# Performance work log

Measured on AMD Instinct MI355X. Metric: run time of the kernel, lower is better.

The kernel has to match this reference:

```python
import jax, jax.numpy as jnp
import numpy as np

DIM = 1024
NUM_HEADS = 8
HEAD_DIM = 128
MAX_SEQ_LEN = 2048
ATTN_SCALE = 0.12
RMS_EPS = 1.1920929e-07  # torch float32 eps (F.rms_norm default)


def rms_norm(x):
    return x * jax.lax.rsqrt(jnp.mean(jnp.square(x), axis=-1, keepdims=True) + RMS_EPS)


def rope_tables(T):
    # angular_freq: (1/1024)**linspace(0,1,head_dim//4), padded with head_dim//4 zeros -> length head_dim//2
    af = (1.0 / 1024.0) ** np.linspace(0.0, 1.0, HEAD_DIM // 4, dtype=np.float32)
    af = np.concatenate([af, np.zeros(HEAD_DIM // 4, dtype=np.float32)])
    t = np.arange(T, dtype=np.float32)
    theta = np.einsum('i,j->ij', t, af)  # [T, head_dim//2]
    return jnp.asarray(np.cos(theta)), jnp.asarray(np.sin(theta))


def apply_rope(x_BTHD, cos, sin):
    # cos/sin: [T, head_dim//2] -> broadcast [1,T,1,hd//2]
    c = cos[None, :, None, :]
    s = sin[None, :, None, :]
    x1, x2 = jnp.split(x_BTHD, 2, axis=-1)
    y1 = x1 * c + x2 * s
    y2 = -x1 * s + x2 * c
    return jnp.concatenate([y1, y2], axis=-1)


def setup_inputs() -> dict:
    key = jax.random.key(0)
    k1, k2, k3, k4, k5 = jax.random.split(key, 5)
    B, T = 4, 2048
    hdim = NUM_HEADS * HEAD_DIM
    std = 0.5 * DIM ** (-0.5)
    bound = (3.0 ** 0.5) * std
    x = jax.random.normal(k1, (B, T, DIM), dtype=jnp.float32)
    ve = jax.random.normal(k2, (B, T, DIM), dtype=jnp.float32)
    sa_lambdas = jax.random.uniform(k3, (2,), dtype=jnp.float32)
    qkv_w = jax.random.uniform(k4, (3, hdim, DIM), dtype=jnp.float32, minval=-bound, maxval=bound)
    # original inits c_proj to zeros; use small random so the output is non-trivial
    c_proj_weight = jax.random.normal(k5, (DIM, hdim), dtype=jnp.float32) * 0.02
    return {"x": x, "ve": ve, "sa_lambdas": sa_lambdas, "qkv_w": qkv_w,
            "c_proj_weight": c_proj_weight}


def reference(x, ve, sa_lambdas, qkv_w, c_proj_weight):
    B, T, D = x.shape
    H, hd = NUM_HEADS, HEAD_DIM
    Wqkv = qkv_w.reshape(3 * H * hd, D)
    qkv = jnp.einsum('btd,ed->bte', x, Wqkv).reshape(B, T, 3 * H, hd)
    q, k, v = jnp.split(qkv, 3, axis=-2)  # each [B,T,H,hd]
    q, k = rms_norm(q), rms_norm(k)
    cos, sin = rope_tables(T)
    q, k = apply_rope(q, cos, sin), apply_rope(k, cos, sin)
    v = sa_lambdas[0] * v + sa_lambdas[1] * ve.reshape(B, T, H, hd)
    # [B,H,T,T] scores
    attn = jnp.einsum('bqhd,bkhd->bhqk', q, k) * ATTN_SCALE
    causal = jnp.triu(jnp.ones((T, T), dtype=bool), k=1)
    attn = jnp.where(causal[None, None], -jnp.inf, attn)
    attn = jax.nn.softmax(attn, axis=-1)
    y = jnp.einsum('bhqk,bkhd->bqhd', attn, v).reshape(B, T, H * hd)
    return jnp.einsum('bte,de->btd', y, c_proj_weight)
```

## Files before the change

kernel.cpp:

```cpp
#include <hip/hip_runtime.h>

#define DIM 1024
#define NH 8
#define HD 128
#define T_SEQ 2048
#define NTOK 8192
#define QKV_N 3072
#define ATTN_SCALE 0.12f
#define RMS_EPS 1.1920929e-07f

using f32x4  = __attribute__((ext_vector_type(4))) float;
using bf16x8 = __attribute__((ext_vector_type(8))) __bf16;

__device__ __forceinline__ unsigned short f2bf(float f) {
    unsigned int u = __builtin_bit_cast(unsigned int, f);
    u += 0x7fffu + ((u >> 16) & 1u);
    return (unsigned short)(u >> 16);
}
__device__ __forceinline__ float bf2f(unsigned short s) {
    unsigned int u = ((unsigned int)s) << 16;
    return __builtin_bit_cast(float, u);
}

__device__ __forceinline__ void gll16(const void* g, void* l) {
    __builtin_amdgcn_global_load_lds(
        (const __attribute__((address_space(1))) unsigned int*)g,
        (__attribute__((address_space(3))) unsigned int*)l, 16, 0, 0);
}

#define VMCNT(n) asm volatile("s_waitcnt vmcnt(" #n ")" ::: "memory")
#define LGKM0 do { asm volatile("s_waitcnt lgkmcnt(0)" ::: "memory"); \
                   __builtin_amdgcn_sched_barrier(0); } while(0)
#define PH_BAR __builtin_amdgcn_s_barrier()

__global__ __launch_bounds__(256) void cvt_f32_bf16(const float* __restrict__ in,
                                                    unsigned short* __restrict__ out,
                                                    int n4) {
    int i = blockIdx.x * 256 + threadIdx.x;
    if (i < n4) {
        float4 f = ((const float4*)in)[i];
        ushort4 o;
        o.x = f2bf(f.x); o.y = f2bf(f.y); o.z = f2bf(f.z); o.w = f2bf(f.w);
        ((ushort4*)out)[i] = o;
    }
}

__global__ __launch_bounds__(256) void rope_tab(float2* __restrict__ tab) {
    int idx = blockIdx.x * 256 + threadIdx.x;
    int t = idx >> 5, i = idx & 31;
    float th = (float)t * exp2f((float)i * (-10.0f/31.0f));
    float sn, cs;
    sincosf(th, &sn, &cs);
    tab[idx] = make_float2(cs, sn);
}

template<int OUTF32>
__global__ __launch_bounds__(512, 1) void gemm8p(const unsigned short* __restrict__ A,
                                                 const unsigned short* __restrict__ B,
                                                 void* __restrict__ Cout,
                                                 int M, int N, int K, int nbn) {
    __shared__ __align__(16) char smem[139264];
    const int tid  = threadIdx.x;
    const int lane = tid & 63;
    const int w    = tid >> 6;
    const int wm   = w >> 2, wn = w & 3;
    const int lr   = lane & 15, lg = lane >> 4;

    const int chunk = gridDim.x >> 3;
    const int bid2  = (blockIdx.x & 7) * chunk + (blockIdx.x >> 3);
    const int bm = (bid2 / nbn) * 256;
    const int bn = (bid2 % nbn) * 256;

    const int srow = lane >> 3;
    const int scol = ((lane & 7) ^ srow) << 3;
    const int KT = K / 64;

    auto ldsA = [&](int p, int h) -> unsigned short* {
        return (unsigned short*)(smem + p*65536 + h*16384);
    };
    auto ldsB = [&](int p, int h) -> unsigned short* {
        return (unsigned short*)(smem + p*65536 + 32768 + h*16384);
    };
    auto stA = [&](int t, int p, int h) {
        if (t >= KT) return;
        char* dst = (char*)ldsA(p, h);
        #pragma unroll
        for (int i = 0; i < 2; ++i) {
            int c = w*2 + i;
            gll16(&A[(size_t)(bm + h*128 + c*8 + srow)*K + t*64 + scol], dst + c*1024);
        }
    };
    auto stB = [&](int t, int p, int h) {
        if (t >= KT) return;
        char* dst = (char*)ldsB(p, h);
        #pragma unroll
        for (int i = 0; i < 2; ++i) {
            int c = w*2 + i;
            gll16(&B[(size_t)(bn + h*128 + c*8 + srow)*K + t*64 + scol], dst + c*1024);
        }
    };

    f32x4 acc[8][4] = {};
    bf16x8 a[4][2], b0[2][2], b1[2][2];

    auto rdA4 = [&](int p, int qm) {
        const unsigned short* base = ldsA(p, wm);
        #pragma unroll
        for (int m = 0; m < 4; ++m) {
            int row = qm*64 + m*16 + lr;
            int sw = (row & 7) << 3;
            #pragma unroll
            for (int kk = 0; kk < 2; ++kk)
                a[m][kk] = *(const bf16x8*)&base[row*64 + ((kk*32 + lg*8) ^ sw)];
        }
    };
    auto rdB2 = [&](int p, int qn, bf16x8 (*bq)[2]) {
        const unsigned short* base = ldsB(p, wn >> 1);
        #pragma unroll
        for (int n = 0; n < 2; ++n) {
            int row = (wn & 1)*64 + qn*32 + n*16 + lr;
            int sw = (row & 7) << 3;
            #pragma unroll
            for (int kk = 0; kk < 2; ++kk)
                bq[n][kk] = *(const bf16x8*)&base[row*64 + ((kk*32 + lg*8) ^ sw)];
        }
    };
    auto mm = [&](int qm, int qn, bf16x8 (*bq)[2]) {
        __builtin_amdgcn_s_setprio(1);
        #pragma unroll
        for (int m = 0; m < 4; ++m)
            #pragma unroll
            for (int n = 0; n < 2; ++n)
                #pragma unroll
                for (int kk = 0; kk < 2; ++kk)
                    acc[qm*4+m][qn*2+n] =
                        __builtin_amdgcn_mfma_f32_16x16x32_bf16(a[m][kk], bq[n][kk],
                                                                acc[qm*4+m][qn*2+n], 0, 0, 0);
        __builtin_amdgcn_s_setprio(0);
    };

    stB(0, 0, 0); stB(0, 0, 1); stA(0, 0, 0); stA(0, 0, 1);
    stB(1, 1, 0); stB(1, 1, 1);
    VMCNT(4);
    PH_BAR;

    for (int i = 0; i < KT/2; ++i) {
        const int t0 = 2*i;
        const bool steady = (i + 1 < KT/2);
        rdA4(0, 0); rdB2(0, 0, b0);
        stA(t0+1, 1, 0);
        PH_BAR; LGKM0;
        mm(0, 0, b0);
        PH_BAR;
        rdB2(0, 1, b1);
        stA(t0+1, 1, 1);
        PH_BAR; LGKM0;
        mm(0, 1, b1);
        PH_BAR;
        rdA4(0, 1);
        stB(t0+2, 0, 0);
        PH_BAR; LGKM0;
        mm(1, 0, b0);
        PH_BAR;
        stB(t0+2, 0, 1);
        if (steady) { VMCNT(4); } else { VMCNT(0); }
        PH_BAR;
        mm(1, 1, b1);
        PH_BAR;
        rdA4(1, 0); rdB2(1, 0, b0);
        stA(t0+2, 0, 0);
        PH_BAR; LGKM0;
        mm(0, 0, b0);
        PH_BAR;
        rdB2(1, 1, b1);
        stA(t0+2, 0, 1);
        PH_BAR; LGKM0;
        mm(0, 1, b1);
        PH_BAR;
        rdA4(1, 1);
        stB(t0+3, 1, 0);
        PH_BAR; LGKM0;
        mm(1, 0, b0);
        PH_BAR;
        stB(t0+3, 1, 1);
        if (steady) { VMCNT(4); } else { VMCNT(0); }
        PH_BAR;
        mm(1, 1, b1);
        PH_BAR;
    }

    __syncthreads();
    float* sc = (float*)(smem + (size_t)w * 17408);
    #pragma unroll
    for (int f = 0; f < 2; ++f) {
        #pragma unroll
        for (int m = 0; m < 4; ++m)
            #pragma unroll
            for (int n = 0; n < 4; ++n)
                #pragma unroll
                for (int r = 0; r < 4; ++r)
                    sc[(m*16 + lg*4 + r)*68 + n*16 + lr] = acc[f*4+m][n][r];
        if (OUTF32) {
            float* C = (float*)Cout;
            #pragma unroll
            for (int rnd = 0; rnd < 16; ++rnd) {
                int g = rnd*64 + lane;
                int row = g >> 4, c4 = (g & 15) * 4;
                float4 v = *(float4*)&sc[row*68 + c4];
                *(float4*)&C[(size_t)(bm + wm*128 + f*64 + row)*N + bn + wn*64 + c4] = v;
            }
        } else {
            unsigned short* C = (unsigned short*)Cout;
            #pragma unroll
            for (int rnd = 0; rnd < 8; ++rnd) {
                int g = rnd*64 + lane;
                int row = g >> 3, c8 = (g & 7) * 8;
                float4 v0 = *(float4*)&sc[row*68 + c8];
                float4 v1 = *(float4*)&sc[row*68 + c8 + 4];
                uint4 o;
                o.x = f2bf(v0.x) | ((unsigned)f2bf(v0.y) << 16);
                o.y = f2bf(v0.z) | ((unsigned)f2bf(v0.w) << 16);
                o.z = f2bf(v1.x) | ((unsigned)f2bf(v1.y) << 16);
                o.w = f2bf(v1.z) | ((unsigned)f2bf(v1.w) << 16);
                *(uint4*)&C[(size_t)(bm + wm*128 + f*64 + row)*N + bn + wn*64 + c8] = o;
            }
        }
    }
}

#define SLOT_A 32768
#define SLOT_SZ 49152

template<int OUTF32>
__global__ __launch_bounds__(512, 1) void gemm256(const unsigned short* __restrict__ A,
                                                  const unsigned short* __restrict__ B,
                                                  void* __restrict__ Cout,
                                                  int M, int N, int K, int nbn) {
    __shared__ __align__(16) char smem[147456];
    const int tid  = threadIdx.x;
    const int lane = tid & 63;
    const int w    = tid >> 6;
    const int wm   = w >> 1, wn = w & 1;
    const int lr   = lane & 15, lg = lane >> 4;
    const int xsw  = (lr & 7) << 3;

    const int chunk = gridDim.x >> 3;
    const int bid2  = (blockIdx.x & 7) * chunk + (blockIdx.x >> 3);
    const int m0 = (bid2 / nbn) * 256;
    const int n0 = (bid2 % nbn) * 128;

    const int rsub = lane >> 3;
    const int csw  = ((lane & 7) ^ rsub) << 3;

    char* s0 = smem;
    char* s1 = smem + SLOT_SZ;
    char* s2 = smem + 2*SLOT_SZ;

    auto stage = [&](int kt, char* slot) {
        const int kb = kt * 64;
        #pragma unroll
        for (int i = 0; i < 4; ++i) {
            int c = w*4 + i;
            gll16(&A[(size_t)(m0 + c*8 + rsub)*K + kb + csw], slot + c*1024);
        }
        #pragma unroll
        for (int i = 0; i < 2; ++i) {
            int c = w*2 + i;
            gll16(&B[(size_t)(n0 + c*8 + rsub)*K + kb + csw], slot + SLOT_A + c*1024);
        }
    };

    f32x4 acc[4][4] = {};
    const int KT = K / 64;

    stage(0, s0);
    stage(1, s1);
    VMCNT(6);
    __builtin_amdgcn_s_barrier();
    __builtin_amdgcn_sched_barrier(0);

    for (int t = 0; t < KT; ++t) {
        if (t + 2 < KT) stage(t + 2, s2);
        const unsigned short* sA = (const unsigned short*)s0;
        const unsigned short* sB = (const unsigned short*)(s0 + SLOT_A);
        bf16x8 bfr[4][2];
        #pragma unroll
        for (int n = 0; n < 4; ++n)
            #pragma unroll
            for (int kk = 0; kk < 2; ++kk)
                bfr[n][kk] = *(const bf16x8*)&sB[(wn*64 + n*16 + lr)*64 + ((kk*32 + lg*8) ^ xsw)];
        #pragma unroll
        for (int m = 0; m < 4; ++m) {
            bf16x8 af[2];
            #pragma unroll
            for (int kk = 0; kk < 2; ++kk)
                af[kk] = *(const bf16x8*)&sA[(wm*64 + m*16 + lr)*64 + ((kk*32 + lg*8) ^ xsw)];
            __builtin_amdgcn_s_setprio(1);
            #pragma unroll
            for (int n = 0; n < 4; ++n)
                #pragma unroll
                for (int kk = 0; kk < 2; ++kk)
                    acc[m][n] = __builtin_amdgcn_mfma_f32_16x16x32_bf16(af[kk], bfr[n][kk], acc[m][n], 0, 0, 0);
            __builtin_amdgcn_s_setprio(0);
        }
        if (t + 2 < KT) { VMCNT(6); }
        else            { VMCNT(0); }
        __builtin_amdgcn_s_barrier();
        __builtin_amdgcn_sched_barrier(0);
        char* tmp = s0; s0 = s1; s1 = s2; s2 = tmp;
    }

    __syncthreads();
    float* sc = (float*)(smem + (size_t)w * 17408);
    #pragma unroll
    for (int m = 0; m < 4; ++m)
        #pragma unroll
        for (int n = 0; n < 4; ++n)
            #pragma unroll
            for (int r = 0; r < 4; ++r)
                sc[(m*16 + lg*4 + r)*68 + n*16 + lr] = acc[m][n][r];

    if (OUTF32) {
        float* C = (float*)Cout;
        #pragma unroll
        for (int rnd = 0; rnd < 16; ++rnd) {
            int g = rnd*64 + lane;
            int row = g >> 4, c4 = (g & 15) * 4;
            float4 v = *(float4*)&sc[row*68 + c4];
            *(float4*)&C[(size_t)(m0 + wm*64 + row)*N + n0 + wn*64 + c4] = v;
        }
    } else {
        unsigned short* C = (unsigned short*)Cout;
        #pragma unroll
        for (int rnd = 0; rnd < 8; ++rnd) {
            int g = rnd*64 + lane;
            int row = g >> 3, c8 = (g & 7) * 8;
            float4 v0 = *(float4*)&sc[row*68 + c8];
            float4 v1 = *(float4*)&sc[row*68 + c8 + 4];
            uint4 o;
            o.x = f2bf(v0.x) | ((unsigned)f2bf(v0.y) << 16);
            o.y = f2bf(v0.z) | ((unsigned)f2bf(v0.w) << 16);
            o.z = f2bf(v1.x) | ((unsigned)f2bf(v1.y) << 16);
            o.w = f2bf(v1.z) | ((unsigned)f2bf(v1.w) << 16);
            *(uint4*)&C[(size_t)(m0 + wm*64 + row)*N + n0 + wn*64 + c8] = o;
        }
    }
}

__global__ __launch_bounds__(256) void qkv_post(const unsigned short* __restrict__ qkv,
                                                const float2* __restrict__ tab,
                                                unsigned short* __restrict__ qO,
                                                unsigned short* __restrict__ kO) {
    int gw   = (blockIdx.x * 256 + threadIdx.x) >> 6;
    int lane = threadIdx.x & 63;
    int h     = gw & 7;
    int token = gw >> 3;
    int t     = token & (T_SEQ-1);
    int b     = token >> 11;

    const unsigned short* base = qkv + (size_t)token * QKV_N + h*HD;
    float q1 = bf2f(base[lane]),        q2 = bf2f(base[lane+64]);
    float k1 = bf2f(base[1024+lane]),   k2 = bf2f(base[1024+lane+64]);

    float sq = q1*q1 + q2*q2;
    float sk = k1*k1 + k2*k2;
    #pragma unroll
    for (int m = 1; m < 64; m <<= 1) {
        sq += __shfl_xor(sq, m);
        sk += __shfl_xor(sk, m);
    }
    float qs = rsqrtf(sq * (1.0f/128.0f) + RMS_EPS) * (ATTN_SCALE * 1.44269504088896f);
    float ks = rsqrtf(sk * (1.0f/128.0f) + RMS_EPS);
    q1 *= qs; q2 *= qs; k1 *= ks; k2 *= ks;

    float cs = 1.0f, sn = 0.0f;
    if (lane < 32) { float2 cc = tab[t*32 + lane]; cs = cc.x; sn = cc.y; }
    float qy1 =  q1*cs + q2*sn, qy2 = -q1*sn + q2*cs;
    float ky1 =  k1*cs + k2*sn, ky2 = -k1*sn + k2*cs;

    size_t obase = ((size_t)(b*NH + h) * T_SEQ + t) * HD;
    qO[obase + lane]      = f2bf(qy1);
    qO[obase + lane + 64] = f2bf(qy2);
    kO[obase + lane]      = f2bf(ky1);
    kO[obase + lane + 64] = f2bf(ky2);
}

__global__ __launch_bounds__(256) void vmix_t(const unsigned short* __restrict__ qkv,
                                              const float* __restrict__ ve,
                                              const float* __restrict__ lam,
                                              unsigned short* __restrict__ vt) {
    __shared__ unsigned short lT[128*72];
    const int tid = threadIdx.x;
    const int t0  = blockIdx.x * 64;
    const int bh  = blockIdx.y;
    const int b = bh >> 3, h = bh & 7;
    const float l0 = lam[0], l1 = lam[1];

    #pragma unroll
    for (int it = 0; it < 4; ++it) {
        int g  = it*256 + tid;
        int t  = g >> 4;
        int d8 = (g & 15) << 3;
        size_t token = (size_t)b*T_SEQ + t0 + t;
        ushort4 v0 = *(const ushort4*)&qkv[token*QKV_N + 2048 + h*HD + d8];
        ushort4 v1 = *(const ushort4*)&qkv[token*QKV_N + 2048 + h*HD + d8 + 4];
        float4 e0 = *(const float4*)&ve[token*DIM + h*HD + d8];
        float4 e1 = *(const float4*)&ve[token*DIM + h*HD + d8 + 4];
        lT[(d8+0)*72 + t] = f2bf(l0*bf2f(v0.x) + l1*e0.x);
        lT[(d8+1)*72 + t] = f2bf(l0*bf2f(v0.y) + l1*e0.y);
        lT[(d8+2)*72 + t] = f2bf(l0*bf2f(v0.z) + l1*e0.z);
        lT[(d8+3)*72 + t] = f2bf(l0*bf2f(v0.w) + l1*e0.w);
        lT[(d8+4)*72 + t] = f2bf(l0*bf2f(v1.x) + l1*e1.x);
        lT[(d8+5)*72 + t] = f2bf(l0*bf2f(v1.y) + l1*e1.y);
        lT[(d8+6)*72 + t] = f2bf(l0*bf2f(v1.z) + l1*e1.z);
        lT[(d8+7)*72 + t] = f2bf(l0*bf2f(v1.w) + l1*e1.w);
    }
    __syncthreads();
    #pragma unroll
    for (int it = 0; it < 4; ++it) {
        int g  = it*256 + tid;
        int d  = g >> 3;
        int t8 = (g & 7) << 3;
        uint4 pk = *(const uint4*)&lT[d*72 + t8];
        *(uint4*)&vt[((size_t)bh*HD + d)*T_SEQ + t0 + t8] = pk;
    }
}

__global__ __launch_bounds__(256, 2) void attn_fwd(const unsigned short* __restrict__ Q,
                                                   const unsigned short* __restrict__ K,
                                                   const unsigned short* __restrict__ Vt,
                                                   unsigned short* __restrict__ Y) {
    __shared__ unsigned short lK[2][64*128];
    __shared__ unsigned short lV[2][128*64];
    __shared__ unsigned short lP[4][16*64];

    const int tid  = threadIdx.x;
    const int lane = tid & 63;
    const int w    = tid >> 6;
    const int lr   = lane & 15, lg = lane >> 4;

    const int lin = blockIdx.y * 16 + blockIdx.x;
    const int bh  = (lin & 7)*4 + ((lin >> 3) & 3);
    const int p   = lin >> 5;
    const int qtA = p, qtB = 31 - p;

    const unsigned short* Qg = Q  + (size_t)bh * T_SEQ * HD;
    const unsigned short* Kg = K  + (size_t)bh * T_SEQ * HD;
    const unsigned short* Vg = Vt + (size_t)bh * HD * T_SEQ;
    const int q0A = qtA*64 + w*16;
    const int q0B = qtB*64 + w*16;

    auto stage = [&](int kt, int s) {
        const int kbase = kt * 64;
        #pragma unroll
        for (int i = 0; i < 4; ++i) {
            int c = w*4 + i;
            int row = c*4 + (lane >> 4);
            int col = ((lane & 15) << 3) ^ ((row & 7) << 3);
            gll16(&Kg[(size_t)(kbase + row)*HD + col], &lK[s][c*512]);
        }
        #pragma unroll
        for (int i = 0; i < 4; ++i) {
            int c = w*4 + i;
            int row = c*8 + (lane >> 3);
            int col = ((lane & 7) << 3) ^ ((row & 7) << 3);
            gll16(&Vg[(size_t)row*T_SEQ + kbase + col], &lV[s][c*512]);
        }
    };

    bf16x8 qfA[4], qfB[4];
    #pragma unroll
    for (int kk = 0; kk < 4; ++kk) {
        qfA[kk] = *(const bf16x8*)&Qg[(size_t)(q0A + lr)*HD + kk*32 + lg*8];
        qfB[kk] = *(const bf16x8*)&Qg[(size_t)(q0B + lr)*HD + kk*32 + lg*8];
    }
    VMCNT(0);
    #pragma unroll
    for (int kk = 0; kk < 4; ++kk)
        asm volatile("" :: "v"(qfA[kk]), "v"(qfB[kk]));

    f32x4 oA[8] = {}, oB[8] = {};
    float psA[4] = {0.f,0.f,0.f,0.f}, psB[4] = {0.f,0.f,0.f,0.f};

    auto passAB = [&](bool diagA, int kbase,
                      const unsigned short* lKc, const unsigned short* lVc) {
        f32x4 sfA[4], sfB[4];
        __builtin_amdgcn_s_setprio(1);
        #pragma unroll
        for (int j = 0; j < 4; ++j) {
            f32x4 sA = {0.f,0.f,0.f,0.f}, sB = {0.f,0.f,0.f,0.f};
            #pragma unroll
            for (int kk = 0; kk < 4; ++kk) {
                bf16x8 kf = *(const bf16x8*)&lKc[(j*16+lr)*128 + ((kk*32 + lg*8) ^ ((lr&7)<<3))];
                sA = __builtin_amdgcn_mfma_f32_16x16x32_bf16(qfA[kk], kf, sA, 0, 0, 0);
                sB = __builtin_amdgcn_mfma_f32_16x16x32_bf16(qfB[kk], kf, sB, 0, 0, 0);
            }
            sfA[j] = sA; sfB[j] = sB;
        }
        __builtin_amdgcn_s_setprio(0);
        if (diagA) {
            #pragma unroll
            for (int j = 0; j < 4; ++j)
                #pragma unroll
                for (int r = 0; r < 4; ++r) {
                    int kcol = kbase + j*16 + lr;
                    int qrow = q0A + lg*4 + r;
                    if (kcol > qrow) sfA[j][r] = -INFINITY;
                }
        }
        #pragma unroll
        for (int j = 0; j < 4; ++j)
            #pragma unroll
            for (int r = 0; r < 4; ++r) {
                float pp = exp2f(sfA[j][r]);
                sfA[j][r] = pp;
                psA[r] += pp;
            }
        asm volatile("" ::: "memory");
        #pragma unroll
        for (int j = 0; j < 4; ++j)
            #pragma unroll
            for (int r = 0; r < 4; ++r) {
                int prow = lg*4 + r;
                lP[w][prow*64 + ((j*16 + lr) ^ ((prow&7)<<3))] = f2bf(sfA[j][r]);
            }
        asm volatile("" ::: "memory");
        bf16x8 pfA[2];
        #pragma unroll
        for (int kk = 0; kk < 2; ++kk)
            pfA[kk] = *(const bf16x8*)&lP[w][lr*64 + ((kk*32 + lg*8) ^ ((lr&7)<<3))];
        #pragma unroll
        for (int j = 0; j < 4; ++j)
            #pragma unroll
            for (int r = 0; r < 4; ++r) {
                float pp = exp2f(sfB[j][r]);
                sfB[j][r] = pp;
                psB[r] += pp;
            }
        asm volatile("" ::: "memory");
        #pragma unroll
        for (int j = 0; j < 4; ++j)
            #pragma unroll
            for (int r = 0; r < 4; ++r) {
                int prow = lg*4 + r;
                lP[w][prow*64 + ((j*16 + lr) ^ ((prow&7)<<3))] = f2bf(sfB[j][r]);
            }
        asm volatile("" ::: "memory");
        bf16x8 pfB[2];
        #pragma unroll
        for (int kk = 0; kk < 2; ++kk)
            pfB[kk] = *(const bf16x8*)&lP[w][lr*64 + ((kk*32 + lg*8) ^ ((lr&7)<<3))];
        #pragma unroll
        for (int n = 0; n < 8; ++n) {
            bf16x8 vf0 = *(const bf16x8*)&lVc[(n*16+lr)*64 + (( 0 + lg*8) ^ ((lr&7)<<3))];
            bf16x8 vf1 = *(const bf16x8*)&lVc[(n*16+lr)*64 + ((32 + lg*8) ^ ((lr&7)<<3))];
            __builtin_amdgcn_s_setprio(1);
            oA[n] = __builtin_amdgcn_mfma_f32_16x16x32_bf16(pfA[0], vf0, oA[n], 0, 0, 0);
            oA[n] = __builtin_amdgcn_mfma_f32_16x16x32_bf16(pfA[1], vf1, oA[n], 0, 0, 0);
            oB[n] = __builtin_amdgcn_mfma_f32_16x16x32_bf16(pfB[0], vf0, oB[n], 0, 0, 0);
            oB[n] = __builtin_amdgcn_mfma_f32_16x16x32_bf16(pfB[1], vf1, oB[n], 0, 0, 0);
            __builtin_amdgcn_s_setprio(0);
        }
    };

    auto pass = [&](bool diag, int kbase,
                    const unsigned short* lKc, const unsigned short* lVc) {
        f32x4 sf[4];
        __builtin_amdgcn_s_setprio(1);
        #pragma unroll
        for (int j = 0; j < 4; ++j) {
            f32x4 s = {0.f,0.f,0.f,0.f};
            #pragma unroll
            for (int kk = 0; kk < 4; ++kk) {
                bf16x8 kf = *(const bf16x8*)&lKc[(j*16+lr)*128 + ((kk*32 + lg*8) ^ ((lr&7)<<3))];
                s = __builtin_amdgcn_mfma_f32_16x16x32_bf16(qfB[kk], kf, s, 0, 0, 0);
            }
            sf[j] = s;
        }
        __builtin_amdgcn_s_setprio(0);
        if (diag) {
            #pragma unroll
            for (int j = 0; j < 4; ++j)
                #pragma unroll
                for (int r = 0; r < 4; ++r) {
                    int kcol = kbase + j*16 + lr;
                    int qrow = q0B + lg*4 + r;
                    if (kcol > qrow) sf[j][r] = -INFINITY;
                }
        }
        #pragma unroll
        for (int j = 0; j < 4; ++j)
            #pragma unroll
            for (int r = 0; r < 4; ++r) {
                float pp = exp2f(sf[j][r]);
                sf[j][r] = pp;
                psB[r] += pp;
            }
        asm volatile("" ::: "memory");
        #pragma unroll
        for (int j = 0; j < 4; ++j)
            #pragma unroll
            for (int r = 0; r < 4; ++r) {
                int prow = lg*4 + r;
                lP[w][prow*64 + ((j*16 + lr) ^ ((prow&7)<<3))] = f2bf(sf[j][r]);
            }
        asm volatile("" ::: "memory");
        bf16x8 pf[2];
        #pragma unroll
        for (int kk = 0; kk < 2; ++kk)
            pf[kk] = *(const bf16x8*)&lP[w][lr*64 + ((kk*32 + lg*8) ^ ((lr&7)<<3))];
        #pragma unroll
        for (int n = 0; n < 8; ++n) {
            bf16x8 vf0 = *(const bf16x8*)&lVc[(n*16+lr)*64 + (( 0 + lg*8) ^ ((lr&7)<<3))];
            bf16x8 vf1 = *(const bf16x8*)&lVc[(n*16+lr)*64 + ((32 + lg*8) ^ ((lr&7)<<3))];
            __builtin_amdgcn_s_setprio(1);
            oB[n] = __builtin_amdgcn_mfma_f32_16x16x32_bf16(pf[0], vf0, oB[n], 0, 0, 0);
            oB[n] = __builtin_amdgcn_mfma_f32_16x16x32_bf16(pf[1], vf1, oB[n], 0, 0, 0);
            __builtin_amdgcn_s_setprio(0);
        }
    };

    stage(0, 0);
    for (int kt = 0; kt <= qtB; ++kt) {
        __builtin_amdgcn_s_barrier();
        const bool pre = (kt + 1 <= qtB);
        if (pre) stage(kt + 1, (kt + 1) & 1);
        if (pre) { VMCNT(8); } else { VMCNT(0); }
        __builtin_amdgcn_sched_barrier(0);
        const int kbase = kt * 64;
        const unsigned short* lKc = lK[kt & 1];
        const unsigned short* lVc = lV[kt & 1];
        if (kt <= qtA) passAB(kt == qtA, kbase, lKc, lVc);
        else           pass(kt == qtB, kbase, lKc, lVc);
    }

    #pragma unroll
    for (int m = 1; m < 16; m <<= 1)
        #pragma unroll
        for (int r = 0; r < 4; ++r) {
            psA[r] += __shfl_xor(psA[r], m);
            psB[r] += __shfl_xor(psB[r], m);
        }
    float riA[4], riB[4];
    #pragma unroll
    for (int r = 0; r < 4; ++r) { riA[r] = 1.0f / psA[r]; riB[r] = 1.0f / psB[r]; }

    const int b = bh >> 3, h = bh & 7;
    #pragma unroll
    for (int n = 0; n < 8; ++n)
        #pragma unroll
        for (int r = 0; r < 4; ++r) {
            int d = n*16 + lr;
            int qrowA = q0A + lg*4 + r;
            int qrowB = q0B + lg*4 + r;
            Y[((size_t)(b*T_SEQ + qrowA))*DIM + h*HD + d] = f2bf(oA[n][r] * riA[r]);
            Y[((size_t)(b*T_SEQ + qrowB))*DIM + h*HD + d] = f2bf(oB[n][r] * riB[r]);
        }
}

extern "C" void kernel_launch(void* const* d_in, const int* in_sizes, int n_in,
                              void* d_out, int out_size, void* d_ws, size_t ws_size,
                              hipStream_t stream) {
    const float* x      = (const float*)d_in[0];
    const float* ve     = (const float*)d_in[1];
    const float* lam    = (const float*)d_in[2];
    const float* qkvw   = (const float*)d_in[3];
    const float* cprojw = (const float*)d_in[4];

    char* ws = (char*)d_ws;
    unsigned short* xb  = (unsigned short*)(ws);
    unsigned short* wqb = (unsigned short*)(ws + 16777216);
    unsigned short* cpb = (unsigned short*)(ws + 23068672);
    unsigned short* qkv = (unsigned short*)(ws + 25165824);
    unsigned short* qa  = (unsigned short*)(ws + 75497472);
    unsigned short* ka  = (unsigned short*)(ws + 92274688);
    unsigned short* vt  = (unsigned short*)(ws + 109051904);
    unsigned short* ya  = (unsigned short*)(ws + 125829120);
    float2* tab = (float2*)(ws);

    cvt_f32_bf16<<<8192, 256, 0, stream>>>(x, xb, 2097152);
    cvt_f32_bf16<<<3072, 256, 0, stream>>>(qkvw, wqb, 786432);
    cvt_f32_bf16<<<1024, 256, 0, stream>>>(cprojw, cpb, 262144);

    gemm8p<0><<<384, 512, 0, stream>>>(xb, wqb, qkv, NTOK, QKV_N, DIM, 12);
    rope_tab<<<256, 256, 0, stream>>>(tab);
    qkv_post<<<16384, 256, 0, stream>>>(qkv, tab, qa, ka);
    vmix_t<<<dim3(32, 32), 256, 0, stream>>>(qkv, ve, lam, vt);
    attn_fwd<<<dim3(16, 32), 256, 0, stream>>>(qa, ka, vt, ya);
    gemm256<1><<<256, 512, 0, stream>>>(ya, cpb, (float*)d_out, NTOK, DIM, DIM, 8);
}
```

Measured before the change: 203.9 us.

## Restructure GEMM pipeline to single-tile stages and transpose attention score layout

The GEMM main loop is reorganised from a two-tile unrolled phase schedule into one K-tile per iteration with double-buffered A fragments. It also allows two blocks per CU via launch bounds and adds a barrier between epilogue halves. The attention kernel computes scores as K·Q^T so each lane holds one query row, which lets P be packed with v_cvt_pk_bf16_f32 into a padded, unswizzled LDS tile. Row sums become a single per-lane accumulator reduced with two shuffles and shared through LDS. The intent is to cut conversion, shuffle and LDS-swizzle overhead, at the risk of more bank conflicts from the padding and register pressure under the new launch bound.

```diff
diff --git a/kernel.cpp b/kernel.cpp
--- a/kernel.cpp
+++ b/kernel.cpp
@@ -21,6 +21,11 @@
     unsigned int u = ((unsigned int)s) << 16;
     return __builtin_bit_cast(float, u);
 }
+__device__ __forceinline__ unsigned int cvtpk(float lo, float hi) {
+    unsigned int r;
+    asm("v_cvt_pk_bf16_f32 %0, %1, %2" : "=v"(r) : "v"(lo), "v"(hi));
+    return r;
+}
 
 __device__ __forceinline__ void gll16(const void* g, void* l) {
     __builtin_amdgcn_global_load_lds(
@@ -29,6 +34,7 @@
 }
 
 #define VMCNT(n) asm volatile("s_waitcnt vmcnt(" #n ")" ::: "memory")
+#define LGKM(n)  asm volatile("s_waitcnt lgkmcnt(" #n ")" ::: "memory")
 #define LGKM0 do { asm volatile("s_waitcnt lgkmcnt(0)" ::: "memory"); \
                    __builtin_amdgcn_sched_barrier(0); } while(0)
 #define PH_BAR __builtin_amdgcn_s_barrier()
@@ -55,7 +61,7 @@
 }
 
 template<int OUTF32>
-__global__ __launch_bounds__(512, 1) void gemm8p(const unsigned short* __restrict__ A,
+__global__ __launch_bounds__(512, 2) void gemm8p(const unsigned short* __restrict__ A,
                                                  const unsigned short* __restrict__ B,
                                                  void* __restrict__ Cout,
                                                  int M, int N, int K, int nbn) {
@@ -71,40 +77,34 @@
     const int bm = (bid2 / nbn) * 256;
     const int bn = (bid2 % nbn) * 256;
 
-    const int srow = lane >> 3;
-    const int scol = ((lane & 7) ^ srow) << 3;
+    const int rsub = lane >> 3;
+    const int csw  = ((lane & 7) ^ rsub) << 3;
     const int KT = K / 64;
 
-    auto ldsA = [&](int p, int h) -> unsigned short* {
-        return (unsigned short*)(smem + p*65536 + h*16384);
-    };
-    auto ldsB = [&](int p, int h) -> unsigned short* {
-        return (unsigned short*)(smem + p*65536 + 32768 + h*16384);
-    };
-    auto stA = [&](int t, int p, int h) {
+    auto stA = [&](int t, int h) {
         if (t >= KT) return;
-        char* dst = (char*)ldsA(p, h);
+        char* dst = smem + (t & 1) * 65536 + h * 16384;
         #pragma unroll
         for (int i = 0; i < 2; ++i) {
             int c = w*2 + i;
-            gll16(&A[(size_t)(bm + h*128 + c*8 + srow)*K + t*64 + scol], dst + c*1024);
-        }
-    };
-    auto stB = [&](int t, int p, int h) {
+            gll16(&A[(size_t)(bm + h*128 + c*8 + rsub)*K + t*64 + csw], dst + c*1024);
+        }
+    };
+    auto stB = [&](int t, int h) {
         if (t >= KT) return;
-        char* dst = (char*)ldsB(p, h);
+        char* dst = smem + (t & 1) * 65536 + 32768 + h * 16384;
         #pragma unroll
         for (int i = 0; i < 2; ++i) {
             int c = w*2 + i;
-            gll16(&B[(size_t)(bn + h*128 + c*8 + srow)*K + t*64 + scol], dst + c*1024);
+            gll16(&B[(size_t)(bn + h*128 + c*8 + rsub)*K + t*64 + csw], dst + c*1024);
         }
     };
 
     f32x4 acc[8][4] = {};
-    bf16x8 a[4][2], b0[2][2], b1[2][2];
-
-    auto rdA4 = [&](int p, int qm) {
-        const unsigned short* base = ldsA(p, wm);
+    bf16x8 a0[4][2], a1[4][2], bb[2][2];
+
+    auto rdA = [&](int t, int qm, bf16x8 (*a)[2]) {
+        const unsigned short* base = (const unsigned short*)(smem + (t & 1)*65536 + wm*16384);
         #pragma unroll
         for (int m = 0; m < 4; ++m) {
             int row = qm*64 + m*16 + lr;
@@ -114,18 +114,18 @@
                 a[m][kk] = *(const bf16x8*)&base[row*64 + ((kk*32 + lg*8) ^ sw)];
         }
     };
-    auto rdB2 = [&](int p, int qn, bf16x8 (*bq)[2]) {
-        const unsigned short* base = ldsB(p, wn >> 1);
+    auto rdB = [&](int t, int qn) {
+        const unsigned short* base = (const unsigned short*)(smem + (t & 1)*65536 + 32768 + (wn >> 1)*16384);
         #pragma unroll
         for (int n = 0; n < 2; ++n) {
             int row = (wn & 1)*64 + qn*32 + n*16 + lr;
             int sw = (row & 7) << 3;
             #pragma unroll
             for (int kk = 0; kk < 2; ++kk)
-                bq[n][kk] = *(const bf16x8*)&base[row*64 + ((kk*32 + lg*8) ^ sw)];
-        }
-    };
-    auto mm = [&](int qm, int qn, bf16x8 (*bq)[2]) {
+                bb[n][kk] = *(const bf16x8*)&base[row*64 + ((kk*32 + lg*8) ^ sw)];
+        }
+    };
+    auto mm = [&](bf16x8 (*a)[2], int qm, int qn) {
         __builtin_amdgcn_s_setprio(1);
         #pragma unroll
         for (int m = 0; m < 4; ++m)
@@ -134,58 +134,37 @@
                 #pragma unroll
                 for (int kk = 0; kk < 2; ++kk)
                     acc[qm*4+m][qn*2+n] =
-                        __builtin_amdgcn_mfma_f32_16x16x32_bf16(a[m][kk], bq[n][kk],
+                        __builtin_amdgcn_mfma_f32_16x16x32_bf16(a[m][kk], bb[n][kk],
                                                                 acc[qm*4+m][qn*2+n], 0, 0, 0);
         __builtin_amdgcn_s_setprio(0);
     };
 
-    stB(0, 0, 0); stB(0, 0, 1); stA(0, 0, 0); stA(0, 0, 1);
-    stB(1, 1, 0); stB(1, 1, 1);
+    stA(0, 0); stA(0, 1); stB(0, 0); stB(0, 1);
+    stA(1, 0); stA(1, 1);
     VMCNT(4);
     PH_BAR;
 
-    for (int i = 0; i < KT/2; ++i) {
-        const int t0 = 2*i;
-        const bool steady = (i + 1 < KT/2);
-        rdA4(0, 0); rdB2(0, 0, b0);
-        stA(t0+1, 1, 0);
+    for (int t = 0; t < KT; ++t) {
+        rdA(t, 0, a0); rdB(t, 0);
+        stB(t + 1, 0);
+        LGKM(8);
         PH_BAR; LGKM0;
-        mm(0, 0, b0);
+        mm(a0, 0, 0);
         PH_BAR;
-        rdB2(0, 1, b1);
-        stA(t0+1, 1, 1);
+        rdA(t, 1, a1);
+        stB(t + 1, 1);
         PH_BAR; LGKM0;
-        mm(0, 1, b1);
+        mm(a1, 1, 0);
         PH_BAR;
-        rdA4(0, 1);
-        stB(t0+2, 0, 0);
+        rdB(t, 1);
+        stA(t + 2, 0);
         PH_BAR; LGKM0;
-        mm(1, 0, b0);
+        mm(a0, 0, 1);
         PH_BAR;
-        stB(t0+2, 0, 1);
-        if (steady) { VMCNT(4); } else { VMCNT(0); }
+        stA(t + 2, 1);
+        if (t + 2 < KT) { VMCNT(4); } else { VMCNT(0); }
         PH_BAR;
-        mm(1, 1, b1);
-        PH_BAR;
-        rdA4(1, 0); rdB2(1, 0, b0);
-        stA(t0+2, 0, 0);
-        PH_BAR; LGKM0;
-        mm(0, 0, b0);
-        PH_BAR;
-        rdB2(1, 1, b1);
-        stA(t0+2, 0, 1);
-        PH_BAR; LGKM0;
-        mm(0, 1, b1);
-        PH_BAR;
-        rdA4(1, 1);
-        stB(t0+3, 1, 0);
-        PH_BAR; LGKM0;
-        mm(1, 0, b0);
-        PH_BAR;
-        stB(t0+3, 1, 1);
-        if (steady) { VMCNT(4); } else { VMCNT(0); }
-        PH_BAR;
-        mm(1, 1, b1);
+        mm(a1, 1, 1);
         PH_BAR;
     }
 
@@ -225,6 +204,7 @@
                 *(uint4*)&C[(size_t)(bm + wm*128 + f*64 + row)*N + bn + wn*64 + c8] = o;
             }
         }
+        if (f == 0) __syncthreads();
     }
 }
 
@@ -432,7 +412,8 @@
                                                    unsigned short* __restrict__ Y) {
     __shared__ unsigned short lK[2][64*128];
     __shared__ unsigned short lV[2][128*64];
-    __shared__ unsigned short lP[4][16*64];
+    __shared__ unsigned short lP[4][16*72];
+    __shared__ float lden[4][2][16];
 
     const int tid  = threadIdx.x;
     const int lane = tid & 63;
@@ -480,7 +461,26 @@
         asm volatile("" :: "v"(qfA[kk]), "v"(qfB[kk]));
 
     f32x4 oA[8] = {}, oB[8] = {};
-    float psA[4] = {0.f,0.f,0.f,0.f}, psB[4] = {0.f,0.f,0.f,0.f};
+    float psA = 0.f, psB = 0.f;
+
+    auto softmax_store = [&](f32x4* sf, float& ps) {
+        #pragma unroll
+        for (int j = 0; j < 4; ++j)
+            #pragma unroll
+            for (int r = 0; r < 4; ++r) {
+                float pp = exp2f(sf[j][r]);
+                sf[j][r] = pp;
+                ps += pp;
+            }
+        #pragma unroll
+        for (int j = 0; j < 4; ++j) {
+            uint2 pk;
+            pk.x = cvtpk(sf[j][0], sf[j][1]);
+            pk.y = cvtpk(sf[j][2], sf[j][3]);
+            *(uint2*)&lP[w][lr*72 + j*16 + lg*4] = pk;
+        }
+        asm volatile("" ::: "memory");
+    };
 
     auto passAB = [&](bool diagA, int kbase,
                       const unsigned short* lKc, const unsigned short* lVc) {
@@ -492,8 +492,8 @@
             #pragma unroll
             for (int kk = 0; kk < 4; ++kk) {
                 bf16x8 kf = *(const bf16x8*)&lKc[(j*16+lr)*128 + ((kk*32 + lg*8) ^ ((lr&7)<<3))];
-                sA = __builtin_amdgcn_mfma_f32_16x16x32_bf16(qfA[kk], kf, sA, 0, 0, 0);
-                sB = __builtin_amdgcn_mfma_f32_16x16x32_bf16(qfB[kk], kf, sB, 0, 0, 0);
+                sA = __builtin_amdgcn_mfma_f32_16x16x32_bf16(kf, qfA[kk], sA, 0, 0, 0);
+                sB = __builtin_amdgcn_mfma_f32_16x16x32_bf16(kf, qfB[kk], sB, 0, 0, 0);
             }
             sfA[j] = sA; sfB[j] = sB;
         }
@@ -503,61 +503,30 @@
             for (int j = 0; j < 4; ++j)
                 #pragma unroll
                 for (int r = 0; r < 4; ++r) {
-                    int kcol = kbase + j*16 + lr;
-                    int qrow = q0A + lg*4 + r;
+                    int kcol = kbase + j*16 + lg*4 + r;
+                    int qrow = q0A + lr;
                     if (kcol > qrow) sfA[j][r] = -INFINITY;
                 }
         }
-        #pragma unroll
-        for (int j = 0; j < 4; ++j)
-            #pragma unroll
-            for (int r = 0; r < 4; ++r) {
-                float pp = exp2f(sfA[j][r]);
-                sfA[j][r] = pp;
-                psA[r] += pp;
-            }
+        softmax_store(sfA, psA);
+        bf16x8 pfA[2];
+        #pragma unroll
+        for (int kk = 0; kk < 2; ++kk)
+            pfA[kk] = *(const bf16x8*)&lP[w][lr*72 + kk*32 + lg*8];
         asm volatile("" ::: "memory");
-        #pragma unroll
-        for (int j = 0; j < 4; ++j)
-            #pragma unroll
-            for (int r = 0; r < 4; ++r) {
-                int prow = lg*4 + r;
-                lP[w][prow*64 + ((j*16 + lr) ^ ((prow&7)<<3))] = f2bf(sfA[j][r]);
-            }
-        asm volatile("" ::: "memory");
-        bf16x8 pfA[2];
+        softmax_store(sfB, psB);
+        bf16x8 pfB[2];
         #pragma unroll
         for (int kk = 0; kk < 2; ++kk)
-            pfA[kk] = *(const bf16x8*)&lP[w][lr*64 + ((kk*32 + lg*8) ^ ((lr&7)<<3))];
-        #pragma unroll
-        for (int j = 0; j < 4; ++j)
-            #pragma unroll
-            for (int r = 0; r < 4; ++r) {
-                float pp = exp2f(sfB[j][r]);
-                sfB[j][r] = pp;
-                psB[r] += pp;
-            }
-        asm volatile("" ::: "memory");
-        #pragma unroll
-        for (int j = 0; j < 4; ++j)
-            #pragma unroll
-            for (int r = 0; r < 4; ++r) {
-                int prow = lg*4 + r;
-                lP[w][prow*64 + ((j*16 + lr) ^ ((prow&7)<<3))] = f2bf(sfB[j][r]);
-            }
-        asm volatile("" ::: "memory");
-        bf16x8 pfB[2];
-        #pragma unroll
-        for (int kk = 0; kk < 2; ++kk)
-            pfB[kk] = *(const bf16x8*)&lP[w][lr*64 + ((kk*32 + lg*8) ^ ((lr&7)<<3))];
+            pfB[kk] = *(const bf16x8*)&lP[w][lr*72 + kk*32 + lg*8];
         #pragma unroll
         for (int n = 0; n < 8; ++n) {
             bf16x8 vf0 = *(const bf16x8*)&lVc[(n*16+lr)*64 + (( 0 + lg*8) ^ ((lr&7)<<3))];
             bf16x8 vf1 = *(const bf16x8*)&lVc[(n*16+lr)*64 + ((32 + lg*8) ^ ((lr&7)<<3))];
             __builtin_amdgcn_s_setprio(1);
             oA[n] = __builtin_amdgcn_mfma_f32_16x16x32_bf16(pfA[0], vf0, oA[n], 0, 0, 0);
+            oB[n] = __builtin_amdgcn_mfma_f32_16x16x32_bf16(pfB[0], vf0, oB[n], 0, 0, 0);
             oA[n] = __builtin_amdgcn_mfma_f32_16x16x32_bf16(pfA[1], vf1, oA[n], 0, 0, 0);
-            oB[n] = __builtin_amdgcn_mfma_f32_16x16x32_bf16(pfB[0], vf0, oB[n], 0, 0, 0);
             oB[n] = __builtin_amdgcn_mfma_f32_16x16x32_bf16(pfB[1], vf1, oB[n], 0, 0, 0);
             __builtin_amdgcn_s_setprio(0);
         }
@@ -573,7 +542,7 @@
             #pragma unroll
             for (int kk = 0; kk < 4; ++kk) {
                 bf16x8 kf = *(const bf16x8*)&lKc[(j*16+lr)*128 + ((kk*32 + lg*8) ^ ((lr&7)<<3))];
-                s = __builtin_amdgcn_mfma_f32_16x16x32_bf16(qfB[kk], kf, s, 0, 0, 0);
+                s = __builtin_amdgcn_mfma_f32_16x16x32_bf16(kf, qfB[kk], s, 0, 0, 0);
             }
             sf[j] = s;
         }
@@ -583,32 +552,16 @@
             for (int j = 0; j < 4; ++j)
                 #pragma unroll
                 for (int r = 0; r < 4; ++r) {
-                    int kcol = kbase + j*16 + lr;
-                    int qrow = q0B + lg*4 + r;
+                    int kcol = kbase + j*16 + lg*4 + r;
+                    int qrow = q0B + lr;
                     if (kcol > qrow) sf[j][r] = -INFINITY;
                 }
         }
-        #pragma unroll
-        for (int j = 0; j < 4; ++j)
-            #pragma unroll
-            for (int r = 0; r < 4; ++r) {
-                float pp = exp2f(sf[j][r]);
-                sf[j][r] = pp;
-                psB[r] += pp;
-            }
-        asm volatile("" ::: "memory");
-        #pragma unroll
-        for (int j = 0; j < 4; ++j)
-            #pragma unroll
-            for (int r = 0; r < 4; ++r) {
-                int prow = lg*4 + r;
-                lP[w][prow*64 + ((j*16 + lr) ^ ((prow&7)<<3))] = f2bf(sf[j][r]);
-            }
-        asm volatile("" ::: "memory");
+        softmax_store(sf, psB);
         bf16x8 pf[2];
         #pragma unroll
         for (int kk = 0; kk < 2; ++kk)
-            pf[kk] = *(const bf16x8*)&lP[w][lr*64 + ((kk*32 + lg*8) ^ ((lr&7)<<3))];
+            pf[kk] = *(const bf16x8*)&lP[w][lr*72 + kk*32 + lg*8];
         #pragma unroll
         for (int n = 0; n < 8; ++n) {
             bf16x8 vf0 = *(const bf16x8*)&lVc[(n*16+lr)*64 + (( 0 + lg*8) ^ ((lr&7)<<3))];
@@ -634,16 +587,16 @@
         else           pass(kt == qtB, kbase, lKc, lVc);
     }
 
-    #pragma unroll
-    for (int m = 1; m < 16; m <<= 1)
-        #pragma unroll
-        for (int r = 0; r < 4; ++r) {
-            psA[r] += __shfl_xor(psA[r], m);
-            psB[r] += __shfl_xor(psB[r], m);
-        }
+    psA += __shfl_xor(psA, 16); psA += __shfl_xor(psA, 32);
+    psB += __shfl_xor(psB, 16); psB += __shfl_xor(psB, 32);
+    if (lane < 16) { lden[w][0][lane] = psA; lden[w][1][lane] = psB; }
+    asm volatile("" ::: "memory");
     float riA[4], riB[4];
     #pragma unroll
-    for (int r = 0; r < 4; ++r) { riA[r] = 1.0f / psA[r]; riB[r] = 1.0f / psB[r]; }
+    for (int r = 0; r < 4; ++r) {
+        riA[r] = 1.0f / lden[w][0][lg*4 + r];
+        riB[r] = 1.0f / lden[w][1][lg*4 + r];
+    }
 
     const int b = bh >> 3, h = bh & 7;
     #pragma unroll
```

After: 193.5 us. 5.1% less time.
